# Kernel tuning notes

Hardware: AMD Instinct MI355X
Metric: run time of the kernel (lower is better)

The kernel has to match this reference:

```python
import jax, jax.numpy as jnp
import numpy as np

OBS_DIM, ACT_DIM, HID_DIM, FEAT = 256, 32, 1024, 512
T_STEPS, BATCH = 64, 512
LOG2PI = float(np.log(2.0 * np.pi))


def _mlp(h, w0, b0, w1, b1, w2, b2):
    # 2 hidden elu layers + linear head (MLPDecoder mean; fix_std Normal, std=1)
    x = jax.nn.elu(h @ w0.T + b0)
    x = jax.nn.elu(x @ w1.T + b1)
    return x @ w2.T + b2


def _gru(x, h, w_ih, w_hh, b_ih, b_hh):
    # torch.nn.GRUCell semantics
    gi = x @ w_ih.T + b_ih
    gh = h @ w_hh.T + b_hh
    i_r, i_z, i_n = jnp.split(gi, 3, axis=-1)
    h_r, h_z, h_n = jnp.split(gh, 3, axis=-1)
    r = jax.nn.sigmoid(i_r + h_r)
    z = jax.nn.sigmoid(i_z + h_z)
    n = jnp.tanh(i_n + r * h_n)
    return (1.0 - z) * n + z * h


def setup_inputs() -> dict:
    key = jax.random.key(0)
    ks = jax.random.split(key, 20)
    d = {}
    d['obs'] = jax.random.normal(ks[0], (T_STEPS, BATCH, OBS_DIM), jnp.float32)
    d['action'] = jax.random.normal(ks[1], (T_STEPS, BATCH, ACT_DIM), jnp.float32)
    d['reward'] = jax.random.normal(ks[2], (T_STEPS, BATCH, 1), jnp.float32)
    in_dim = OBS_DIM + ACT_DIM
    s = lambda fan_in: 1.0 / np.sqrt(fan_in)
    d['gru_w_ih'] = jax.random.normal(ks[3], (3 * HID_DIM, in_dim), jnp.float32) * s(in_dim)
    d['gru_w_hh'] = jax.random.normal(ks[4], (3 * HID_DIM, HID_DIM), jnp.float32) * s(HID_DIM)
    d['gru_b_ih'] = jnp.zeros((3 * HID_DIM,), jnp.float32)
    d['gru_b_hh'] = jnp.zeros((3 * HID_DIM,), jnp.float32)
    for name, out_dim, base in (('obs', OBS_DIM, 5), ('rew', 1, 11)):
        d[f'{name}_w0'] = jax.random.normal(ks[base], (FEAT, HID_DIM), jnp.float32) * s(HID_DIM)
        d[f'{name}_b0'] = jnp.zeros((FEAT,), jnp.float32)
        d[f'{name}_w1'] = jax.random.normal(ks[base + 1], (FEAT, FEAT), jnp.float32) * s(FEAT)
        d[f'{name}_b1'] = jnp.zeros((FEAT,), jnp.float32)
        d[f'{name}_w2'] = jax.random.normal(ks[base + 2], (out_dim, FEAT), jnp.float32) * s(FEAT)
        d[f'{name}_b2'] = jnp.zeros((out_dim,), jnp.float32)
    return d


def reference(obs, action, reward,
              gru_w_ih, gru_w_hh, gru_b_ih, gru_b_hh,
              obs_w0, obs_b0, obs_w1, obs_b1, obs_w2, obs_b2,
              rew_w0, rew_b0, rew_w1, rew_b1, rew_w2, rew_b2):
    T, B = obs.shape[0], obs.shape[1]

    def normal_logprob_sum(x, mean):
        # Normal(mean, std=1): -0.5*(x-mean)^2 - 0.5*log(2*pi), summed
        return -0.5 * jnp.sum((x - mean) ** 2 + LOG2PI)

    h0 = _gru(jnp.concatenate([obs[0], jnp.zeros_like(action[0])], axis=1),
              jnp.zeros((B, HID_DIM), obs.dtype),
              gru_w_ih, gru_w_hh, gru_b_ih, gru_b_hh)

    def step(h, xs):
        obs_t, act_t, rew_t = xs
        obs_mean = _mlp(h, obs_w0, obs_b0, obs_w1, obs_b1, obs_w2, obs_b2)
        lp_obs = normal_logprob_sum(obs_t, obs_mean)
        rew_mean = _mlp(h, rew_w0, rew_b0, rew_w1, rew_b1, rew_w2, rew_b2)
        lp_rew = normal_logprob_sum(rew_t, rew_mean)
        # feed predicted obs (mode) + ground-truth action back into the GRU
        x = jnp.concatenate([obs_mean, act_t], axis=1)
        h_next = _gru(x, h, gru_w_ih, gru_w_hh, gru_b_ih, gru_b_hh)
        return h_next, (obs_mean, rew_mean, lp_obs, lp_rew)

    _, (pre_obs, pre_reward, lp_obs, lp_rew) = jax.lax.scan(
        step, h0, (obs, action, reward))

    denom = jnp.asarray(T * B, obs.dtype)
    pre_obs_loss = -jnp.sum(lp_obs) / denom
    pre_reward_loss = -jnp.sum(lp_rew) / denom
    loss = pre_obs_loss + pre_reward_loss  # action_mimic=False -> action loss is 0
    return loss, pre_obs, pre_reward
```

## Files before the change

kernel.cpp:

```cpp
#include <hip/hip_runtime.h>
#include <stdint.h>

#define T_STEPS 64
#define BATCH   512
#define OBS_DIM 256
#define ACT_DIM 32
#define HID     1024
#define FEAT    512
#define GDIM    3072
#define KIH     288
#define NBLK    256
#define GMEMB   32
#define LOG2PI  1.8378770664093453f
#define HWREG_XCC_ID 14356

typedef __attribute__((ext_vector_type(8))) short  short8;
typedef __attribute__((ext_vector_type(4))) float  floatx4;
typedef __attribute__((ext_vector_type(4))) unsigned int uintx4;
typedef unsigned long long ull;

__device__ __forceinline__ float bf2f(unsigned int u) {
    return __uint_as_float(u << 16);
}
__device__ __forceinline__ unsigned int f2bf(float f) {
    unsigned int u = __float_as_uint(f);
    return (u + 0x7FFFu + ((u >> 16) & 1u)) >> 16;
}
__device__ __forceinline__ float elu1(float x)  { return x > 0.f ? x : expm1f(x); }
__device__ __forceinline__ float sigm(float x)  { return 1.f / (1.f + expf(-x)); }

__device__ __forceinline__ unsigned int dev_ld(const unsigned int* p) {
    return __hip_atomic_load(p, __ATOMIC_RELAXED, __HIP_MEMORY_SCOPE_AGENT);
}
__device__ __forceinline__ ull dev_ld64(const ull* p) {
    return __hip_atomic_load(p, __ATOMIC_RELAXED, __HIP_MEMORY_SCOPE_AGENT);
}
__device__ __forceinline__ void dev_st(unsigned int* p, unsigned int v) {
    __hip_atomic_store(p, v, __ATOMIC_RELAXED, __HIP_MEMORY_SCOPE_AGENT);
}
__device__ __forceinline__ float dev_ldf(const float* p) {
    return __uint_as_float(dev_ld((const unsigned int*)p));
}

template<bool COH>
__device__ __forceinline__ unsigned int a_ld(const unsigned int* p) {
    return COH ? dev_ld(p) : *p;
}
template<bool COH>
__device__ __forceinline__ ull a_ld64(const ull* p) {
    return COH ? dev_ld64(p) : *p;
}
template<bool COH>
__device__ __forceinline__ void a_st(unsigned int* p, unsigned int v) {
    if (COH) dev_st(p, v); else *p = v;
}

struct ParamsReal {
    const float* obs; const float* action; const float* reward;
    const float* b_ih; const float* b_hh;
    const float* b1o; const float* b1r; const float* b2o; const float* b2r;
    const unsigned short* Ws1; const unsigned short* Wih;
    const unsigned short* W1o; const unsigned short* W1r;
    const unsigned short* W2o; const unsigned short* w2r;
    const float* bias_s1;
    unsigned short* Z1[2]; unsigned short* Z2[2]; unsigned short* Xbuf[2];
    unsigned short* hbf[2]; unsigned short* GHb[2]; float* h[2];
    float* accum; float* out;
    int* bar;
};
#define P ParamsReal

__device__ __forceinline__ void bar_fast() {
    asm volatile("" ::: "memory");
    __builtin_amdgcn_s_barrier();
    asm volatile("" ::: "memory");
}
__device__ __forceinline__ void bar_lds() {
    asm volatile("s_waitcnt lgkmcnt(0)" ::: "memory");
    __builtin_amdgcn_s_barrier();
    asm volatile("" ::: "memory");
}

__device__ __forceinline__ void gbar(int* cnt, int* gen, int& epoch, int members) {
    __syncthreads();
    if (threadIdx.x == 0) {
        __builtin_amdgcn_fence(__ATOMIC_RELEASE, "workgroup");
        epoch++;
        int prev = __hip_atomic_fetch_add(cnt, 1, __ATOMIC_RELAXED,
                                          __HIP_MEMORY_SCOPE_AGENT);
        if (prev == members * epoch - 1) {
            __hip_atomic_store(gen, epoch, __ATOMIC_RELAXED,
                               __HIP_MEMORY_SCOPE_AGENT);
        } else {
            while (__hip_atomic_load(gen, __ATOMIC_RELAXED,
                                     __HIP_MEMORY_SCOPE_AGENT) < epoch)
                __builtin_amdgcn_s_sleep(2);
        }
        __builtin_amdgcn_fence(__ATOMIC_ACQUIRE, "workgroup");
    }
    __syncthreads();
}

__device__ __forceinline__ void gbar_flags(int* fbase, int m, int& epoch) {
    __syncthreads();
    epoch++;
    if (threadIdx.x == 0) {
        __builtin_amdgcn_fence(__ATOMIC_RELEASE, "workgroup");
        dev_st((unsigned int*)(fbase + m * 16), (unsigned int)epoch);
    }
    if (threadIdx.x < 64) {
        const unsigned int* fp =
            (const unsigned int*)(fbase + (threadIdx.x & 31) * 16);
        while ((int)dev_ld(fp) < epoch) __builtin_amdgcn_s_sleep(1);
        __builtin_amdgcn_fence(__ATOMIC_ACQUIRE, "workgroup");
    }
    __syncthreads();
}

template<bool COH>
__device__ __forceinline__ void s1_stage(const P& p, unsigned short* lds,
                                         int g, int m,
                                         const unsigned short* hbf_r,
                                         unsigned short* Z1_w,
                                         unsigned short* GHb_w) {
    const int tid = threadIdx.x, lane = tid & 63, wv = tid >> 6;
    const int wr = wv & 1, wc = wv >> 1, fr = lane & 15, fq = lane >> 4;
    const int rowg = g * 64, col0 = m * 128;
    unsigned short* ldsA = lds;
    unsigned short* ldsB = lds + 64 * 136;

    floatx4 acc[2][4];
    floatx4 z4 = {0.f, 0.f, 0.f, 0.f};
#pragma unroll
    for (int mi = 0; mi < 2; ++mi)
#pragma unroll
        for (int n = 0; n < 4; ++n) acc[mi][n] = z4;

    const ull* Aq = (const ull*)(hbf_r + (size_t)rowg * HID);
    const unsigned short* Bg = p.Ws1 + (size_t)col0 * HID;

    ull apf[8];
#pragma unroll
    for (int j = 0; j < 8; ++j) { int f = tid + 256 * j;
        apf[j] = a_ld64<COH>(Aq + (size_t)(f >> 5) * 256 + (f & 31)); }
    uintx4 rb0[4], rb1[4];
#pragma unroll
    for (int i = 0; i < 4; ++i) { int c = tid + 256 * i;
        const unsigned short* bp = Bg + (size_t)(c >> 3) * HID + ((c & 7) << 3);
        rb0[i] = __builtin_nontemporal_load((const uintx4*)bp);
        rb1[i] = __builtin_nontemporal_load((const uintx4*)(bp + 64)); }

#define S1_MFMA(ASUB)                                                          \
    {                                                                          \
        _Pragma("unroll")                                                      \
        for (int ks = 0; ks < 2; ++ks) {                                       \
            short8 af[2], bf8[4];                                              \
            _Pragma("unroll")                                                  \
            for (int mi = 0; mi < 2; ++mi)                                     \
                af[mi] = *(const short8*)(ldsA + (wr * 32 + mi * 16 + fr) * 136 + (ASUB) + ks * 32 + fq * 8); \
            _Pragma("unroll")                                                  \
            for (int n = 0; n < 4; ++n)                                        \
                bf8[n] = *(const short8*)(ldsB + (wc * 64 + n * 16 + fr) * 72 + ks * 32 + fq * 8); \
            _Pragma("unroll")                                                  \
            for (int mi = 0; mi < 2; ++mi)                                     \
                _Pragma("unroll")                                              \
                for (int n = 0; n < 4; ++n)                                    \
                    acc[mi][n] = __builtin_amdgcn_mfma_f32_16x16x32_bf16(      \
                        af[mi], bf8[n], acc[mi][n], 0, 0, 0);                  \
        }                                                                      \
    }

    for (int it2 = 0; it2 < 8; ++it2) {
        bar_fast();
#pragma unroll
        for (int j = 0; j < 8; ++j) { int f = tid + 256 * j;
            *(ull*)(ldsA + (size_t)(f >> 5) * 136 + ((f & 31) << 2)) = apf[j]; }
#pragma unroll
        for (int i = 0; i < 4; ++i) { int c = tid + 256 * i;
            *(uintx4*)(ldsB + (c >> 3) * 72 + ((c & 7) << 3)) = rb0[i]; }
        bar_lds();
        if (it2 < 7) {
            int c2 = it2 + 1;
#pragma unroll
            for (int j = 0; j < 8; ++j) { int f = tid + 256 * j;
                apf[j] = a_ld64<COH>(Aq + (size_t)(f >> 5) * 256 + c2 * 32 + (f & 31)); }
            int k0n = (2 * it2 + 2) * 64;
#pragma unroll
            for (int i = 0; i < 4; ++i) { int c = tid + 256 * i;
                rb0[i] = __builtin_nontemporal_load((const uintx4*)
                    (Bg + (size_t)(c >> 3) * HID + k0n + ((c & 7) << 3))); }
        }
        S1_MFMA(0);
        bar_fast();
#pragma unroll
        for (int i = 0; i < 4; ++i) { int c = tid + 256 * i;
            *(uintx4*)(ldsB + (c >> 3) * 72 + ((c & 7) << 3)) = rb1[i]; }
        bar_lds();
        if (it2 < 7) {
            int k0n = (2 * it2 + 3) * 64;
#pragma unroll
            for (int i = 0; i < 4; ++i) { int c = tid + 256 * i;
                rb1[i] = __builtin_nontemporal_load((const uintx4*)
                    (Bg + (size_t)(c >> 3) * HID + k0n + ((c & 7) << 3))); }
        }
        S1_MFMA(64);
    }
#undef S1_MFMA

    const bool isZ1 = (col0 < 1024);
#pragma unroll
    for (int mi = 0; mi < 2; ++mi)
#pragma unroll
        for (int n = 0; n < 4; ++n)
#pragma unroll
            for (int j = 0; j < 4; ++j) {
                int row = rowg + wr * 32 + mi * 16 + fq * 4 + j;
                int col = col0 + wc * 64 + n * 16 + fr;
                float v = acc[mi][n][j] + p.bias_s1[col];
                unsigned int ow = f2bf(isZ1 ? elu1(v) : v);
                unsigned int pr = __shfl_xor(ow, 1, 64);
                if (!(fr & 1)) {
                    unsigned int pk = ow | (pr << 16);
                    if (isZ1)
                        a_st<COH>((unsigned int*)(Z1_w + row * HID + col), pk);
                    else
                        a_st<COH>((unsigned int*)GHb_w + (size_t)row * 1536 + ((col - 1024) >> 1), pk);
                }
            }
}

template<bool COH>
__device__ __forceinline__ void s2_stage(const P& p, unsigned short* lds,
                                         int g, int m,
                                         const unsigned short* Z1_r,
                                         unsigned short* Z2_w) {
    const int tid = threadIdx.x, lane = tid & 63, wv = tid >> 6;
    const int wr = wv & 1, wc = wv >> 1, fr = lane & 15, fq = lane >> 4;
    const int rowg = g * 64;
    const int z = m >> 4, col0 = (m & 15) * 32;
    unsigned short* ldsA = lds;
    unsigned short* ldsB = lds + 64 * 136;

    floatx4 acc[2];
    floatx4 z4 = {0.f, 0.f, 0.f, 0.f};
    acc[0] = z4; acc[1] = z4;

    const ull* Aq = (const ull*)(Z1_r + (size_t)rowg * HID + z * FEAT);
    const unsigned short* Bg = (z ? p.W1r : p.W1o) + (size_t)col0 * FEAT;
    const float* bias = z ? p.b1r : p.b1o;

    ull apf[8];
#pragma unroll
    for (int j = 0; j < 8; ++j) { int f = tid + 256 * j;
        apf[j] = a_ld64<COH>(Aq + (size_t)(f >> 5) * 256 + (f & 31)); }
    const unsigned short* bp0 = Bg + (size_t)(tid >> 3) * FEAT + ((tid & 7) << 3);
    uintx4 rb0 = *(const uintx4*)(bp0);
    uintx4 rb1 = *(const uintx4*)(bp0 + 64);

#define S23_MFMA(ASUB)                                                         \
    { _Pragma("unroll")                                                        \
      for (int ks = 0; ks < 2; ++ks) {                                         \
        short8 bf8 = *(const short8*)(ldsB + (wc * 16 + fr) * 72 + ks * 32 + fq * 8); \
        _Pragma("unroll")                                                      \
        for (int mi = 0; mi < 2; ++mi) {                                       \
            short8 af = *(const short8*)(ldsA + (wr * 32 + mi * 16 + fr) * 136 + (ASUB) + ks * 32 + fq * 8); \
            acc[mi] = __builtin_amdgcn_mfma_f32_16x16x32_bf16(af, bf8, acc[mi], 0, 0, 0); \
        }                                                                      \
      } }

    for (int it2 = 0; it2 < 4; ++it2) {
        bar_fast();
#pragma unroll
        for (int j = 0; j < 8; ++j) { int f = tid + 256 * j;
            *(ull*)(ldsA + (size_t)(f >> 5) * 136 + ((f & 31) << 2)) = apf[j]; }
        *(uintx4*)(ldsB + (tid >> 3) * 72 + ((tid & 7) << 3)) = rb0;
        bar_lds();
        if (it2 < 3) {
            int c2 = it2 + 1;
#pragma unroll
            for (int j = 0; j < 8; ++j) { int f = tid + 256 * j;
                apf[j] = a_ld64<COH>(Aq + (size_t)(f >> 5) * 256 + c2 * 32 + (f & 31)); }
            rb0 = *(const uintx4*)(bp0 + (2 * it2 + 2) * 64);
        }
        S23_MFMA(0);
        bar_fast();
        *(uintx4*)(ldsB + (tid >> 3) * 72 + ((tid & 7) << 3)) = rb1;
        bar_lds();
        if (it2 < 3) rb1 = *(const uintx4*)(bp0 + (2 * it2 + 3) * 64);
        S23_MFMA(64);
    }

#pragma unroll
    for (int mi = 0; mi < 2; ++mi)
#pragma unroll
        for (int j = 0; j < 4; ++j) {
            int row = rowg + wr * 32 + mi * 16 + fq * 4 + j;
            int col = col0 + wc * 16 + fr;
            float v = acc[mi][j] + bias[col];
            unsigned int ow = f2bf(elu1(v));
            unsigned int pr = __shfl_xor(ow, 1, 64);
            if (!(fr & 1))
                a_st<COH>((unsigned int*)(Z2_w + row * HID + z * FEAT + col), ow | (pr << 16));
        }
}

template<bool COH>
__device__ __forceinline__ void s3_stage(const P& p, unsigned short* lds,
                                         int g, int m, int t,
                                         const unsigned short* Z2_r,
                                         unsigned short* Xbuf_w) {
    const int tid = threadIdx.x, lane = tid & 63, wv = tid >> 6;
    const int wr = wv & 1, wc = wv >> 1;
    const int fr = lane & 15, fq = lane >> 4;
    const int rowg = g * 64;

    if (m < 8) {
        const int col0 = m * 32;
        unsigned short* ldsA = lds;
        unsigned short* ldsB = lds + 64 * 136;
        floatx4 acc[2];
        floatx4 z4 = {0.f, 0.f, 0.f, 0.f};
        acc[0] = z4; acc[1] = z4;

        const ull* Aq = (const ull*)(Z2_r + (size_t)rowg * HID);
        const unsigned short* Bg = p.W2o + (size_t)col0 * FEAT;

        ull apf[8];
#pragma unroll
        for (int j = 0; j < 8; ++j) { int f = tid + 256 * j;
            apf[j] = a_ld64<COH>(Aq + (size_t)(f >> 5) * 256 + (f & 31)); }
        const unsigned short* bp0 = Bg + (size_t)(tid >> 3) * FEAT + ((tid & 7) << 3);
        uintx4 rb0 = *(const uintx4*)(bp0);
        uintx4 rb1 = *(const uintx4*)(bp0 + 64);

        for (int it2 = 0; it2 < 4; ++it2) {
            bar_fast();
#pragma unroll
            for (int j = 0; j < 8; ++j) { int f = tid + 256 * j;
                *(ull*)(ldsA + (size_t)(f >> 5) * 136 + ((f & 31) << 2)) = apf[j]; }
            *(uintx4*)(ldsB + (tid >> 3) * 72 + ((tid & 7) << 3)) = rb0;
            bar_lds();
            if (it2 < 3) {
                int c2 = it2 + 1;
#pragma unroll
                for (int j = 0; j < 8; ++j) { int f = tid + 256 * j;
                    apf[j] = a_ld64<COH>(Aq + (size_t)(f >> 5) * 256 + c2 * 32 + (f & 31)); }
                rb0 = *(const uintx4*)(bp0 + (2 * it2 + 2) * 64);
            }
            S23_MFMA(0);
            bar_fast();
            *(uintx4*)(ldsB + (tid >> 3) * 72 + ((tid & 7) << 3)) = rb1;
            bar_lds();
            if (it2 < 3) rb1 = *(const uintx4*)(bp0 + (2 * it2 + 3) * 64);
            S23_MFMA(64);
        }

        const int col = col0 + wc * 16 + fr;
        const float b2oc = p.b2o[col];
        float lsum = 0.f;
#pragma unroll
        for (int mi = 0; mi < 2; ++mi)
#pragma unroll
            for (int j = 0; j < 4; ++j) {
                int row = rowg + wr * 32 + mi * 16 + fq * 4 + j;
                float mval = acc[mi][j] + b2oc;
                size_t oidx = (size_t)t * BATCH * OBS_DIM + (size_t)row * OBS_DIM + col;
                __builtin_nontemporal_store(mval, p.out + 1 + oidx);
                unsigned int ow = f2bf(mval);
                unsigned int pr = __shfl_xor(ow, 1, 64);
                if (!(fr & 1))
                    a_st<COH>((unsigned int*)(Xbuf_w + row * KIH + col), ow | (pr << 16));
                float d = __builtin_nontemporal_load(p.obs + oidx) - mval;
                lsum += d * d;
            }
#pragma unroll
        for (int off = 32; off > 0; off >>= 1) lsum += __shfl_down(lsum, off, 64);
        if (lane == 0) atomicAdd(p.accum + 0, lsum);
    } else if (m == 8) {
        for (int e = tid; e < 64 * 16; e += 256) {
            int row = rowg + (e >> 4), cp = (e & 15) * 2;
            const float* ap = p.action + ((size_t)t * BATCH + row) * ACT_DIM + cp;
            unsigned int lo = f2bf(__builtin_nontemporal_load(ap));
            unsigned int hi = f2bf(__builtin_nontemporal_load(ap + 1));
            a_st<COH>((unsigned int*)(Xbuf_w + row * KIH + OBS_DIM + cp), lo | (hi << 16));
        }
    } else if (m >= 16) {
        const int row = rowg + (m - 16) * 4 + wv;
        const ull* zq = (const ull*)(Z2_r + (size_t)row * HID + FEAT) + lane * 2;
        ull z0 = a_ld64<COH>(zq);
        ull z1 = a_ld64<COH>(zq + 1);
        short8 w8 = *(const short8*)(p.w2r + lane * 8);
        float s = 0.f;
#pragma unroll
        for (int k = 0; k < 4; ++k) {
            unsigned int u = (unsigned int)(z0 >> (16 * k)) & 0xFFFFu;
            s += bf2f(u) * bf2f((unsigned int)(unsigned short)w8[k]);
        }
#pragma unroll
        for (int k = 0; k < 4; ++k) {
            unsigned int u = (unsigned int)(z1 >> (16 * k)) & 0xFFFFu;
            s += bf2f(u) * bf2f((unsigned int)(unsigned short)w8[4 + k]);
        }
#pragma unroll
        for (int off = 32; off > 0; off >>= 1) s += __shfl_down(s, off, 64);
        if (lane == 0) {
            float mm = s + p.b2r[0];
            __builtin_nontemporal_store(
                mm, p.out + 1 + (size_t)T_STEPS * BATCH * OBS_DIM + (size_t)t * BATCH + row);
            float d = __builtin_nontemporal_load(p.reward + (size_t)t * BATCH + row) - mm;
            atomicAdd(p.accum + 1, d * d);
        }
    }
}

template<bool COH>
__device__ __forceinline__ void s4_stage(const P& p, unsigned short* lds,
                                         int g, int m, int use_gh,
                                         const unsigned short* Xbuf_r,
                                         const unsigned short* GHb_r,
                                         const float* h_r,
                                         float* h_w, unsigned short* hbf_w) {
    const int tid = threadIdx.x, lane = tid & 63, wv = tid >> 6;
    const int wr = wv & 1, wc = wv >> 1;
    const int fr = lane & 15, fq = lane >> 4;
    const int rowg = g * 64;
    const int col0 = m * 32;
    unsigned short* ldsA = lds;
    unsigned short* ldsB = lds + 64 * 104;

    floatx4 acc[3][2];
    floatx4 z4 = {0.f, 0.f, 0.f, 0.f};
#pragma unroll
    for (int g3 = 0; g3 < 3; ++g3) { acc[g3][0] = z4; acc[g3][1] = z4; }

    const ull* Xq = (const ull*)(Xbuf_r + (size_t)rowg * KIH);
    ull apf[6];
#pragma unroll
    for (int j = 0; j < 6; ++j) { int f = tid + 256 * j;
        apf[j] = a_ld64<COH>(Xq + (size_t)(f / 24) * 72 + (f % 24)); }

    uintx4 wpfA[5], wpfB[5];
#pragma unroll
    for (int j = 0; j < 5; ++j) { int f = tid + 256 * j;
        if (f < 1152) { int r = f / 12, ko = (f - r * 12) * 8;
            const unsigned short* wp =
                p.Wih + (size_t)((r >> 5) * HID + col0 + (r & 31)) * KIH + ko;
            wpfA[j] = __builtin_nontemporal_load((const uintx4*)wp);
            wpfB[j] = __builtin_nontemporal_load((const uintx4*)(wp + 96)); } }

#pragma unroll
    for (int c = 0; c < 3; ++c) {
        bar_fast();
#pragma unroll
        for (int j = 0; j < 6; ++j) { int f = tid + 256 * j;
            *(ull*)(ldsA + (size_t)(f / 24) * 104 + ((f % 24) << 2)) = apf[j]; }
#pragma unroll
        for (int j = 0; j < 5; ++j) { int f = tid + 256 * j;
            if (f < 1152) { int r = f / 12, ko = (f - r * 12) * 8;
                *(uintx4*)(ldsB + r * 104 + ko) = (c & 1) ? wpfB[j] : wpfA[j]; } }
        bar_lds();
        if (c < 2) {
#pragma unroll
            for (int j = 0; j < 6; ++j) { int f = tid + 256 * j;
                apf[j] = a_ld64<COH>(Xq + (size_t)(f / 24) * 72 + (c + 1) * 24 + (f % 24)); }
        }
        if (c == 0) {
#pragma unroll
            for (int j = 0; j < 5; ++j) { int f = tid + 256 * j;
                if (f < 1152) { int r = f / 12, ko = (f - r * 12) * 8;
                    wpfA[j] = __builtin_nontemporal_load((const uintx4*)
                        (p.Wih + (size_t)((r >> 5) * HID + col0 + (r & 31)) * KIH + 192 + ko)); } }
        }
#pragma unroll
        for (int ks = 0; ks < 3; ++ks) {
            short8 af[2];
#pragma unroll
            for (int mi = 0; mi < 2; ++mi)
                af[mi] = *(const short8*)(ldsA + (wr * 32 + mi * 16 + fr) * 104 + ks * 32 + fq * 8);
#pragma unroll
            for (int g3 = 0; g3 < 3; ++g3) {
                short8 bf8 = *(const short8*)(ldsB + (g3 * 32 + wc * 16 + fr) * 104 + ks * 32 + fq * 8);
#pragma unroll
                for (int mi = 0; mi < 2; ++mi)
                    acc[g3][mi] = __builtin_amdgcn_mfma_f32_16x16x32_bf16(
                        af[mi], bf8, acc[g3][mi], 0, 0, 0);
            }
        }
    }

    const int col = col0 + wc * 16 + fr;
    const float bir = p.b_ih[col];
    const float biz = p.b_ih[HID + col];
    const float bin = p.b_ih[2 * HID + col];
    float hrv[2][4], hzv[2][4], hnv[2][4], hpv[2][4];
    if (use_gh) {
        const unsigned int* GW = (const unsigned int*)GHb_r;
        const int cw = col >> 1, hi = col & 1;
#pragma unroll
        for (int mi = 0; mi < 2; ++mi)
#pragma unroll
            for (int j = 0; j < 4; ++j) {
                int row = rowg + wr * 32 + mi * 16 + fq * 4 + j;
                unsigned int ur = a_ld<COH>(GW + (size_t)row * 1536 + cw);
                unsigned int uz = a_ld<COH>(GW + (size_t)row * 1536 + 512 + cw);
                unsigned int un = a_ld<COH>(GW + (size_t)row * 1536 + 1024 + cw);
                hrv[mi][j] = bf2f(hi ? (ur >> 16) : (ur & 0xFFFFu));
                hzv[mi][j] = bf2f(hi ? (uz >> 16) : (uz & 0xFFFFu));
                hnv[mi][j] = bf2f(hi ? (un >> 16) : (un & 0xFFFFu));
                hpv[mi][j] = __uint_as_float(a_ld<COH>((const unsigned int*)(h_r + (size_t)row * HID + col)));
            }
    } else {
        float br = p.b_hh[col], bz = p.b_hh[HID + col], bn = p.b_hh[2 * HID + col];
#pragma unroll
        for (int mi = 0; mi < 2; ++mi)
#pragma unroll
            for (int j = 0; j < 4; ++j) {
                hrv[mi][j] = br; hzv[mi][j] = bz; hnv[mi][j] = bn; hpv[mi][j] = 0.f;
            }
    }
#pragma unroll
    for (int mi = 0; mi < 2; ++mi)
#pragma unroll
        for (int j = 0; j < 4; ++j) {
            int row = rowg + wr * 32 + mi * 16 + fq * 4 + j;
            float r  = sigm(acc[0][mi][j] + bir + hrv[mi][j]);
            float z  = sigm(acc[1][mi][j] + biz + hzv[mi][j]);
            float nn = tanhf(acc[2][mi][j] + bin + r * hnv[mi][j]);
            float hv = (1.f - z) * nn + z * hpv[mi][j];
            a_st<COH>((unsigned int*)(h_w + (size_t)row * HID + col), __float_as_uint(hv));
            unsigned int ow = f2bf(hv);
            unsigned int pr = __shfl_xor(ow, 1, 64);
            if (!(fr & 1))
                a_st<COH>((unsigned int*)(hbf_w + row * HID + col), ow | (pr << 16));
        }
}

template<bool COH>
__device__ void rollout(const P& p, unsigned short* lds, int g, int m) {
    int* fbase = p.bar + 2048 + g * 512;
    int fep = 0;

    s4_stage<COH>(p, lds, g, m, 0, p.Xbuf[1], p.GHb[0], p.h[0], p.h[0], p.hbf[0]);
    gbar_flags(fbase, m, fep);

    for (int t = 0; t < T_STEPS; ++t) {
        const int pr = t & 1, nx = (t + 1) & 1;
        s1_stage<COH>(p, lds, g, m, p.hbf[pr], p.Z1[pr], p.GHb[pr]);
        gbar_flags(fbase, m, fep);
        s2_stage<COH>(p, lds, g, m, p.Z1[pr], p.Z2[pr]);
        gbar_flags(fbase, m, fep);
        s3_stage<COH>(p, lds, g, m, t, p.Z2[pr], p.Xbuf[pr]);
        gbar_flags(fbase, m, fep);
        if (t < T_STEPS - 1) {
            s4_stage<COH>(p, lds, g, m, 1, p.Xbuf[pr], p.GHb[pr], p.h[pr],
                          p.h[nx], p.hbf[nx]);
            gbar_flags(fbase, m, fep);
        }
    }
}

__global__ __launch_bounds__(256, 1) void k_persist(P p) {
    __shared__ unsigned short lds[17920];
    __shared__ int sh[3];

    const int bid = blockIdx.x;
    if (threadIdx.x == 0) {
        unsigned int xcd = __builtin_amdgcn_s_getreg(HWREG_XCC_ID) & 7u;
        int r = __hip_atomic_fetch_add(p.bar + 1024 + xcd, 1,
                                       __ATOMIC_RELAXED, __HIP_MEMORY_SCOPE_AGENT);
        sh[0] = (int)xcd; sh[1] = r;
    }
    int repoch = 0;
    gbar(p.bar + 1200, p.bar + 1264, repoch, NBLK);
    if (threadIdx.x == 0) {
        int ok = (sh[1] < 32);
        for (int i = 0; i < 8; ++i)
            ok &= (dev_ld((const unsigned int*)(p.bar + 1024 + i)) == 32u);
        sh[2] = ok;
    }
    __syncthreads();

    if (sh[2]) rollout<false>(p, lds, sh[0], sh[1]);
    else       rollout<true >(p, lds, bid & 7, bid >> 3);

    gbar(p.bar + 1200, p.bar + 1264, repoch, NBLK);
    if (bid == 0 && threadIdx.x == 0) {
        const float inv = 1.f / (float)(T_STEPS * BATCH);
        float a0 = dev_ldf(p.accum + 0);
        float a1 = dev_ldf(p.accum + 1);
        p.out[0] = 0.5f * a0 * inv + 128.f * LOG2PI
                 + 0.5f * a1 * inv + 0.5f * LOG2PI;
    }
}

__global__ void k_convert(
    const float* __restrict__ ow0, const float* __restrict__ rw0,
    const float* __restrict__ whh, const float* __restrict__ wih,
    const float* __restrict__ ow1, const float* __restrict__ rw1,
    const float* __restrict__ ow2, const float* __restrict__ rw2,
    const float* __restrict__ ob0, const float* __restrict__ rb0,
    const float* __restrict__ bhh,
    unsigned short* __restrict__ Ws1, unsigned short* __restrict__ Wih,
    unsigned short* __restrict__ W1o, unsigned short* __restrict__ W1r,
    unsigned short* __restrict__ W2o, unsigned short* __restrict__ w2r,
    float* __restrict__ bias_s1)
{
    const int i0 = blockIdx.x * 256 + threadIdx.x;
    const int stride = gridDim.x * 256;
    for (int i = i0; i < 4096 * 1024; i += stride) {
        int row = i >> 10;
        float v = (row < 512) ? ow0[i]
                : (row < 1024) ? rw0[i - 512 * 1024]
                               : whh[i - 1024 * 1024];
        Ws1[i] = (unsigned short)f2bf(v);
    }
    for (int i = i0; i < GDIM * KIH; i += stride) Wih[i] = (unsigned short)f2bf(wih[i]);
    for (int i = i0; i < FEAT * FEAT; i += stride) {
        W1o[i] = (unsigned short)f2bf(ow1[i]);
        W1r[i] = (unsigned short)f2bf(rw1[i]);
    }
    for (int i = i0; i < OBS_DIM * FEAT; i += stride) W2o[i] = (unsigned short)f2bf(ow2[i]);
    for (int i = i0; i < FEAT; i += stride) w2r[i] = (unsigned short)f2bf(rw2[i]);
    for (int i = i0; i < 4096; i += stride)
        bias_s1[i] = (i < 512) ? ob0[i] : (i < 1024) ? rb0[i - 512] : bhh[i - 1024];
}

__global__ void k_init(const float* __restrict__ obs,
                       unsigned short* __restrict__ Xbuf1,
                       float* __restrict__ accum,
                       int* __restrict__ bar)
{
    int i = blockIdx.x * 256 + threadIdx.x;
    if (i < BATCH * KIH) {
        int row = i / KIH, col = i - row * KIH;
        Xbuf1[i] = (col < OBS_DIM) ? (unsigned short)f2bf(obs[row * OBS_DIM + col])
                                   : (unsigned short)0;
    }
    if (i < 2)    accum[i] = 0.f;
    if (i < 8192) bar[i] = 0;
}

extern "C" void kernel_launch(void* const* d_in, const int* in_sizes, int n_in,
                              void* d_out, int out_size, void* d_ws, size_t ws_size,
                              hipStream_t stream)
{
    const float* obs      = (const float*)d_in[0];
    const float* action   = (const float*)d_in[1];
    const float* reward   = (const float*)d_in[2];
    const float* gru_w_ih = (const float*)d_in[3];
    const float* gru_w_hh = (const float*)d_in[4];
    const float* gru_b_ih = (const float*)d_in[5];
    const float* gru_b_hh = (const float*)d_in[6];
    const float* obs_w0   = (const float*)d_in[7];
    const float* obs_b0   = (const float*)d_in[8];
    const float* obs_w1   = (const float*)d_in[9];
    const float* obs_b1   = (const float*)d_in[10];
    const float* obs_w2   = (const float*)d_in[11];
    const float* obs_b2   = (const float*)d_in[12];
    const float* rew_w0   = (const float*)d_in[13];
    const float* rew_b0   = (const float*)d_in[14];
    const float* rew_w1   = (const float*)d_in[15];
    const float* rew_b1   = (const float*)d_in[16];
    const float* rew_w2   = (const float*)d_in[17];
    const float* rew_b2   = (const float*)d_in[18];

    char* ws = (char*)d_ws;
    auto alloc = [&](size_t bytes) -> char* {
        char* pr = ws;
        ws += (bytes + 255) & ~(size_t)255;
        return pr;
    };
    unsigned short* Ws1  = (unsigned short*)alloc((size_t)4096 * 1024 * 2);
    unsigned short* Wih  = (unsigned short*)alloc((size_t)GDIM * KIH * 2);
    unsigned short* W1o  = (unsigned short*)alloc((size_t)FEAT * FEAT * 2);
    unsigned short* W1r  = (unsigned short*)alloc((size_t)FEAT * FEAT * 2);
    unsigned short* W2o  = (unsigned short*)alloc((size_t)OBS_DIM * FEAT * 2);
    unsigned short* w2r  = (unsigned short*)alloc((size_t)FEAT * 2);
    float* bias_s1       = (float*)alloc((size_t)4096 * 4);
    unsigned short* Z1a  = (unsigned short*)alloc((size_t)BATCH * HID * 2);
    unsigned short* Z1b  = (unsigned short*)alloc((size_t)BATCH * HID * 2);
    unsigned short* Z2a  = (unsigned short*)alloc((size_t)BATCH * HID * 2);
    unsigned short* Z2b  = (unsigned short*)alloc((size_t)BATCH * HID * 2);
    unsigned short* GHa  = (unsigned short*)alloc((size_t)BATCH * GDIM * 2);
    unsigned short* GHbB = (unsigned short*)alloc((size_t)BATCH * GDIM * 2);
    unsigned short* Xba  = (unsigned short*)alloc((size_t)BATCH * KIH * 2);
    unsigned short* Xbb  = (unsigned short*)alloc((size_t)BATCH * KIH * 2);
    float* ha            = (float*)alloc((size_t)BATCH * HID * 4);
    float* hb            = (float*)alloc((size_t)BATCH * HID * 4);
    unsigned short* hfa  = (unsigned short*)alloc((size_t)BATCH * HID * 2);
    unsigned short* hfb  = (unsigned short*)alloc((size_t)BATCH * HID * 2);
    float* accum         = (float*)alloc(256);
    int*   bar           = (int*)alloc(32768);

    k_convert<<<dim3(1024), dim3(256), 0, stream>>>(
        obs_w0, rew_w0, gru_w_hh, gru_w_ih, obs_w1, rew_w1, obs_w2, rew_w2,
        obs_b0, rew_b0, gru_b_hh, Ws1, Wih, W1o, W1r, W2o, w2r, bias_s1);

    k_init<<<dim3((BATCH * KIH + 255) / 256), dim3(256), 0, stream>>>(obs, Xbb, accum, bar);

    P hp;
    hp.obs = obs; hp.action = action; hp.reward = reward;
    hp.b_ih = gru_b_ih; hp.b_hh = gru_b_hh;
    hp.b1o = obs_b1; hp.b1r = rew_b1; hp.b2o = obs_b2; hp.b2r = rew_b2;
    hp.Ws1 = Ws1; hp.Wih = Wih; hp.W1o = W1o; hp.W1r = W1r;
    hp.W2o = W2o; hp.w2r = w2r; hp.bias_s1 = bias_s1;
    hp.Z1[0] = Z1a; hp.Z1[1] = Z1b;
    hp.Z2[0] = Z2a; hp.Z2[1] = Z2b;
    hp.Xbuf[0] = Xba; hp.Xbuf[1] = Xbb;
    hp.hbf[0] = hfa; hp.hbf[1] = hfb;
    hp.GHb[0] = GHa; hp.GHb[1] = GHbB;
    hp.h[0] = ha; hp.h[1] = hb;
    hp.accum = accum; hp.out = (float*)d_out;
    hp.bar = bar;

    k_persist<<<dim3(NBLK), dim3(256), 0, stream>>>(hp);
}
```

Baseline: 2.495 ms.

## Replace full group barriers with dependency-selective flag waits between rollout stages

Each intra-group barrier now waits only on the flags of the member blocks whose outputs the next stage actually reads, using per-stage masks, instead of on all 32 members. The barrier before the GRU stage also checks that other members have finished an earlier phase, using an older epoch target. This is meant to cut straggler wait time per timestep. It relies on the masks matching the real data dependencies exactly; a wrong mask would create a race.

```diff
diff --git a/kernel.cpp b/kernel.cpp
--- a/kernel.cpp
+++ b/kernel.cpp
@@ -101,17 +101,29 @@
     __syncthreads();
 }
 
-__device__ __forceinline__ void gbar_flags(int* fbase, int m, int& epoch) {
+__device__ __forceinline__ void gbar_sel(int* fbase, int m, int& epoch,
+                                         unsigned int mask_now,
+                                         unsigned int mask_old, int old_back) {
     __syncthreads();
     epoch++;
     if (threadIdx.x == 0) {
         __builtin_amdgcn_fence(__ATOMIC_RELEASE, "workgroup");
         dev_st((unsigned int*)(fbase + m * 16), (unsigned int)epoch);
     }
-    if (threadIdx.x < 64) {
-        const unsigned int* fp =
-            (const unsigned int*)(fbase + (threadIdx.x & 31) * 16);
-        while ((int)dev_ld(fp) < epoch) __builtin_amdgcn_s_sleep(1);
+    const int lane = threadIdx.x;
+    if (lane < 32) {
+        if ((mask_now >> lane) & 1u) {
+            const unsigned int* fp = (const unsigned int*)(fbase + lane * 16);
+            while ((int)dev_ld(fp) < epoch) __builtin_amdgcn_s_sleep(1);
+        }
+        __builtin_amdgcn_fence(__ATOMIC_ACQUIRE, "workgroup");
+    } else if (lane < 64) {
+        const int l2 = lane - 32;
+        if ((mask_old >> l2) & 1u) {
+            const unsigned int* fp = (const unsigned int*)(fbase + l2 * 16);
+            const int tgt = epoch - old_back;
+            while ((int)dev_ld(fp) < tgt) __builtin_amdgcn_s_sleep(1);
+        }
         __builtin_amdgcn_fence(__ATOMIC_ACQUIRE, "workgroup");
     }
     __syncthreads();
@@ -539,22 +551,24 @@
 __device__ void rollout(const P& p, unsigned short* lds, int g, int m) {
     int* fbase = p.bar + 2048 + g * 512;
     int fep = 0;
+    const unsigned int m2mask = (m < 8) ? 0x0000FFFFu
+                              : (m >= 16 ? 0xFFFF0000u : 0u);
 
     s4_stage<COH>(p, lds, g, m, 0, p.Xbuf[1], p.GHb[0], p.h[0], p.h[0], p.hbf[0]);
-    gbar_flags(fbase, m, fep);
+    gbar_sel(fbase, m, fep, 0xFFFFFFFFu, 0u, 0);
 
     for (int t = 0; t < T_STEPS; ++t) {
         const int pr = t & 1, nx = (t + 1) & 1;
         s1_stage<COH>(p, lds, g, m, p.hbf[pr], p.Z1[pr], p.GHb[pr]);
-        gbar_flags(fbase, m, fep);
+        gbar_sel(fbase, m, fep, 0x000000FFu, 0u, 0);
         s2_stage<COH>(p, lds, g, m, p.Z1[pr], p.Z2[pr]);
-        gbar_flags(fbase, m, fep);
+        gbar_sel(fbase, m, fep, m2mask, 0u, 0);
         s3_stage<COH>(p, lds, g, m, t, p.Z2[pr], p.Xbuf[pr]);
-        gbar_flags(fbase, m, fep);
         if (t < T_STEPS - 1) {
+            gbar_sel(fbase, m, fep, 0x000001FFu, 0xFFFFFE00u, 2);
             s4_stage<COH>(p, lds, g, m, 1, p.Xbuf[pr], p.GHb[pr], p.h[pr],
                           p.h[nx], p.hbf[nx]);
-            gbar_flags(fbase, m, fep);
+            gbar_sel(fbase, m, fep, 0xFFFFFFFFu, 0u, 0);
         }
     }
 }
```

New measurement: 2.507 ms. Within noise of the previous version (+0.5%).
